# Performance work log

Hardware: AMD Instinct MI355X
Metric: run time of the kernel (lower is better)

## Reference

```python
import jax, jax.numpy as jnp
import numpy as np

NUM_FEATURES = 81   # atom feature width used in matmuls
N_NODES = 262144
N_COLS = 103        # num_features + num_bond
OUT_CH = 128
COORD = 3           # distance rule slice [0:3]


def setup_inputs() -> dict:
    key = jax.random.key(0)
    k1, k2, k3, k4 = jax.random.split(key, 4)
    features = jax.random.normal(k1, (N_NODES, N_COLS), dtype=jnp.float32)
    # columns 81, 82 hold neighbor indices (0 => no neighbor), stored as floats
    idx = jax.random.randint(k4, (N_NODES, 2), 0, N_NODES).astype(jnp.float32)
    features = features.at[:, NUM_FEATURES:NUM_FEATURES + 2].set(idx)
    w_s = jax.random.normal(k2, (NUM_FEATURES, OUT_CH), dtype=jnp.float32) * 0.05
    w_n = jax.random.normal(k3, (N_COLS, OUT_CH), dtype=jnp.float32) * 0.05
    return {"features": features, "w_s": w_s, "w_n": w_n}


def reference(features, w_s, w_n):
    F = NUM_FEATURES
    self_f = features[:, :F]                       # [N, F]
    new_features = self_f @ w_s                    # [N, C] self term

    idx0 = features[:, F].astype(jnp.int32)        # neighbor slot 0
    idx1 = features[:, F + 1].astype(jnp.int32)    # neighbor slot 1

    def neighbor_contrib(idx):
        nei = features[idx]                                        # gather [N, 103]
        # rule 0: 'distance' over [0:COORD] -> keep neighbor slice, record distance
        d = jnp.sqrt(jnp.sum(jnp.square(self_f[:, :COORD] - nei[:, :COORD]), axis=-1))
        seg_dist = nei[:, :COORD]                                  # [N, 3]
        # rule 1: 'sum' over [COORD:F]
        seg_sum = self_f[:, COORD:F] + nei[:, COORD:F]             # [N, F-3]
        comb = jnp.concatenate([seg_dist, seg_sum], axis=-1)       # [N, F]
        d_eff = jnp.where(d > 0, d, jnp.float32(0.01))
        comb = comb / jnp.square(d_eff)[:, None]                   # distance scaling
        return comb @ w_n[:F] + new_features                       # tiny-matmul batched

    c0 = neighbor_contrib(idx0)
    c1 = neighbor_contrib(idx1)
    # rows with no valid neighbor were never written -> zeros
    out = jnp.where((idx1 != 0)[:, None], c1,
                    jnp.where((idx0 != 0)[:, None], c0, jnp.float32(0.0)))
    return out
```

## Files before the change

### kernel.cpp

```cpp
#include <hip/hip_runtime.h>
#include <hip/hip_bf16.h>

constexpr int kNodes = 262144;
constexpr int NC  = 103;
constexpr int F   = 81;
constexpr int OC  = 128;
constexpr int NKS = 6;
constexpr int NPB = 64;
constexpr int THREADS = 256;
constexpr int NST = 96;
constexpr int SELF_F4 = NPB * NC / 4;

typedef __attribute__((ext_vector_type(8))) short bf16x8;
typedef __attribute__((ext_vector_type(4))) float f32x4;

__device__ inline ushort f2bf(float f) {
  uint u = __float_as_uint(f);
  return (ushort)((u + 0x7fffu + ((u >> 16) & 1u)) >> 16);
}
__device__ inline short bfc(float x) {
  return (short)__bfloat16_as_ushort(__float2bfloat16(x));
}

__device__ __forceinline__ void gll4(const float* g, float* l) {
  __builtin_amdgcn_global_load_lds(
      (const __attribute__((address_space(1))) unsigned int*)g,
      (__attribute__((address_space(3))) unsigned int*)l, 4, 0, 0);
}
__device__ __forceinline__ void gll16(const float* g, float* l) {
  __builtin_amdgcn_global_load_lds(
      (const __attribute__((address_space(1))) unsigned int*)g,
      (__attribute__((address_space(3))) unsigned int*)l, 16, 0, 0);
}

__global__ __launch_bounds__(256)
void prep_w(const float* __restrict__ w_s, const float* __restrict__ w_n,
            ushort* __restrict__ wf) {
  int t = blockIdx.x * 256 + threadIdx.x;
  if (t >= NKS * 8 * 64) return;
  int l  = t & 63;
  int ct = (t >> 6) & 7;
  int ks = t >> 9;
  int c  = ct * 16 + (l & 15);
  int kb = ks * 32 + ((l >> 4) << 3);
  union { ushort u[8]; int4 v; } o;
  #pragma unroll
  for (int i = 0; i < 8; ++i) {
    int k = kb + i;
    float f = 0.f;
    if (k < F)                      f = w_s[k * OC + c];
    else if (k >= 96 && k < 96 + F) f = w_n[(k - 96) * OC + c];
    o.u[i] = f2bf(f);
  }
  ((int4*)wf)[t] = o.v;
}

__global__ __launch_bounds__(THREADS)
void rgc_v13(const float* __restrict__ feat, const ushort* __restrict__ wf,
             float* __restrict__ out) {
  __shared__ __align__(16) float lds_self[NPB * NC];
  __shared__ __align__(16) float lds_nei[NPB * NST];
  __shared__ int   s_sel[NPB];
  __shared__ float s_cs[NPB];

  const int tid = threadIdx.x;
  const int w   = tid >> 6;
  const int l   = tid & 63;
  const long base = (long)blockIdx.x * NPB;
  const float* fbase = feat + base * NC;

  const bf16x8* wfv = (const bf16x8*)wf;
  bf16x8 bA[NKS], bB[NKS];
  #pragma unroll
  for (int ks = 0; ks < NKS; ++ks) {
    bA[ks] = wfv[(ks * 8 + w)     * 64 + l];
    bB[ks] = wfv[(ks * 8 + w + 4) * 64 + l];
  }

  #pragma unroll
  for (int j = 0; j < 7; ++j) {
    int i = tid + j * THREADS;
    if (j < 6 || i < SELF_F4) {
      gll16((const float*)((const float4*)fbase + i),
            (float*)((float4*)lds_self + (j * THREADS + w * 64)));
    }
  }
  if (l < 16) {
    const int n = w * 16 + l;
    const float* row = feat + (base + n) * NC;
    float f0 = row[F], f1 = row[F + 1];
    int i0 = (int)f0, i1 = (int)f1;
    s_sel[n] = (i1 != 0) ? i1 : i0;
  }
  asm volatile("s_waitcnt lgkmcnt(0)" ::: "memory");
  __builtin_amdgcn_s_barrier();

  #pragma unroll
  for (int j = 0; j < 24; ++j) {
    int v   = tid + j * THREADS;
    int row = v / NST;
    int p   = v - row * NST;
    int c   = p >> 5;
    int x   = (p >> 2) & 7;
    int cl  = p & 3;
    int col = (c << 5) + ((x ^ (row & 7)) << 2) + cl;
    gll4(feat + (long)s_sel[row] * NC + col,
         lds_nei + (j * THREADS + w * 64));
  }
  asm volatile("s_waitcnt vmcnt(0) lgkmcnt(0)" ::: "memory");
  __builtin_amdgcn_s_barrier();

  if (tid < NPB) {
    const int n = tid;
    const int r = n & 7;
    float nx = lds_nei[n * NST + r * 4 + 0];
    float ny = lds_nei[n * NST + r * 4 + 1];
    float nz = lds_nei[n * NST + r * 4 + 2];
    float dx = lds_self[n * NC + 0] - nx;
    float dy = lds_self[n * NC + 1] - ny;
    float dz = lds_self[n * NC + 2] - nz;
    float d2 = dx * dx + dy * dy + dz * dz;
    float alive = (s_sel[n] != 0) ? 1.f : 0.f;
    s_cs[n] = alive * ((d2 > 0.f) ? (1.f / d2) : 10000.f);
  }
  asm volatile("s_waitcnt lgkmcnt(0)" ::: "memory");
  __builtin_amdgcn_s_barrier();

  const int q    = l >> 4;
  const int lrow = l & 15;
  const int off0 = q * 8;
  const int col  = l & 15;

  #pragma unroll
  for (int nt = 0; nt < 4; ++nt) {
    const int n = nt * 16 + lrow;
    const int r = n & 7;
    const float* sp = lds_self + n * NC;
    const float* np = lds_nei + n * NST;
    const float alive = (s_sel[n] != 0) ? 1.f : 0.f;
    const float cs    = s_cs[n];

    bf16x8 afS[3], afC[3];
    #pragma unroll
    for (int c = 0; c < 3; ++c) {
      f32x4 lo = *(const f32x4*)(np + c * 32 + (((2 * q)     ^ r) << 2));
      f32x4 hi = *(const f32x4*)(np + c * 32 + (((2 * q + 1) ^ r) << 2));
      #pragma unroll
      for (int i = 0; i < 8; ++i) {
        float sv = sp[c * 32 + off0 + i];
        float nv = (i < 4) ? lo[i] : hi[i - 4];
        afS[c][i] = bfc(sv * alive);
        float se = sv;
        if (c == 0 && i < 3 && q == 0) se = 0.f;
        afC[c][i] = bfc((nv + se) * cs);
      }
    }

    f32x4 a0 = (f32x4)(0.f), a1 = (f32x4)(0.f);
    #pragma unroll
    for (int ks = 0; ks < NKS; ++ks) {
      bf16x8 af = (ks < 3) ? afS[ks] : afC[ks - 3];
      a0 = __builtin_amdgcn_mfma_f32_16x16x32_bf16(af, bA[ks], a0, 0, 0, 0);
      a1 = __builtin_amdgcn_mfma_f32_16x16x32_bf16(af, bB[ks], a1, 0, 0, 0);
    }

    const long orow = base + nt * 16 + q * 4;
    #pragma unroll
    for (int rr = 0; rr < 4; ++rr) {
      out[(orow + rr) * OC + w * 16       + col] = a0[rr];
      out[(orow + rr) * OC + (w + 4) * 16 + col] = a1[rr];
    }
  }
}

extern "C" void kernel_launch(void* const* d_in, const int* in_sizes, int n_in,
                              void* d_out, int out_size, void* d_ws, size_t ws_size,
                              hipStream_t stream) {
  const float* feat = (const float*)d_in[0];
  const float* w_s  = (const float*)d_in[1];
  const float* w_n  = (const float*)d_in[2];
  float* outp = (float*)d_out;
  ushort* wf = (ushort*)d_ws;

  prep_w<<<dim3((NKS * 8 * 64 + 255) / 256), 256, 0, stream>>>(w_s, w_n, wf);
  rgc_v13<<<dim3(kNodes / NPB), THREADS, 0, stream>>>(feat, wf, outp);
}
```

Before: 67.75 us.

## Read self rows directly from global into registers, drop self LDS staging

Removes the LDS staging buffer for the block's own feature rows. Each lane now loads its 24 self features straight from global memory as unaligned 4-wide vectors, and computes the distance scale per lane instead of in a separate pass with an extra barrier. This cuts LDS footprint, which may raise occupancy, and removes one barrier phase. The cost is uncoalesced, redundant global reads of the self rows, since four waves read the same rows, and the node-tile loop is no longer unrolled.

```diff
diff --git a/kernel.cpp b/kernel.cpp
--- a/kernel.cpp
+++ b/kernel.cpp
@@ -9,10 +9,10 @@
 constexpr int NPB = 64;
 constexpr int THREADS = 256;
 constexpr int NST = 96;
-constexpr int SELF_F4 = NPB * NC / 4;
 
 typedef __attribute__((ext_vector_type(8))) short bf16x8;
 typedef __attribute__((ext_vector_type(4))) float f32x4;
+typedef float f32x4u __attribute__((ext_vector_type(4))) __attribute__((aligned(4)));
 
 __device__ inline ushort f2bf(float f) {
   uint u = __float_as_uint(f);
@@ -26,11 +26,6 @@
   __builtin_amdgcn_global_load_lds(
       (const __attribute__((address_space(1))) unsigned int*)g,
       (__attribute__((address_space(3))) unsigned int*)l, 4, 0, 0);
-}
-__device__ __forceinline__ void gll16(const float* g, float* l) {
-  __builtin_amdgcn_global_load_lds(
-      (const __attribute__((address_space(1))) unsigned int*)g,
-      (__attribute__((address_space(3))) unsigned int*)l, 16, 0, 0);
 }
 
 __global__ __launch_bounds__(256)
@@ -56,18 +51,15 @@
 }
 
 __global__ __launch_bounds__(THREADS)
-void rgc_v13(const float* __restrict__ feat, const ushort* __restrict__ wf,
+void rgc_v14(const float* __restrict__ feat, const ushort* __restrict__ wf,
              float* __restrict__ out) {
-  __shared__ __align__(16) float lds_self[NPB * NC];
   __shared__ __align__(16) float lds_nei[NPB * NST];
-  __shared__ int   s_sel[NPB];
-  __shared__ float s_cs[NPB];
+  __shared__ int s_sel[NPB];
 
   const int tid = threadIdx.x;
   const int w   = tid >> 6;
   const int l   = tid & 63;
   const long base = (long)blockIdx.x * NPB;
-  const float* fbase = feat + base * NC;
 
   const bf16x8* wfv = (const bf16x8*)wf;
   bf16x8 bA[NKS], bB[NKS];
@@ -77,14 +69,6 @@
     bB[ks] = wfv[(ks * 8 + w + 4) * 64 + l];
   }
 
-  #pragma unroll
-  for (int j = 0; j < 7; ++j) {
-    int i = tid + j * THREADS;
-    if (j < 6 || i < SELF_F4) {
-      gll16((const float*)((const float4*)fbase + i),
-            (float*)((float4*)lds_self + (j * THREADS + w * 64)));
-    }
-  }
   if (l < 16) {
     const int n = w * 16 + l;
     const float* row = feat + (base + n) * NC;
@@ -107,23 +91,7 @@
     gll4(feat + (long)s_sel[row] * NC + col,
          lds_nei + (j * THREADS + w * 64));
   }
-  asm volatile("s_waitcnt vmcnt(0) lgkmcnt(0)" ::: "memory");
-  __builtin_amdgcn_s_barrier();
-
-  if (tid < NPB) {
-    const int n = tid;
-    const int r = n & 7;
-    float nx = lds_nei[n * NST + r * 4 + 0];
-    float ny = lds_nei[n * NST + r * 4 + 1];
-    float nz = lds_nei[n * NST + r * 4 + 2];
-    float dx = lds_self[n * NC + 0] - nx;
-    float dy = lds_self[n * NC + 1] - ny;
-    float dz = lds_self[n * NC + 2] - nz;
-    float d2 = dx * dx + dy * dy + dz * dz;
-    float alive = (s_sel[n] != 0) ? 1.f : 0.f;
-    s_cs[n] = alive * ((d2 > 0.f) ? (1.f / d2) : 10000.f);
-  }
-  asm volatile("s_waitcnt lgkmcnt(0)" ::: "memory");
+  asm volatile("s_waitcnt vmcnt(0)" ::: "memory");
   __builtin_amdgcn_s_barrier();
 
   const int q    = l >> 4;
@@ -131,14 +99,29 @@
   const int off0 = q * 8;
   const int col  = l & 15;
 
-  #pragma unroll
+  #pragma unroll 1
   for (int nt = 0; nt < 4; ++nt) {
     const int n = nt * 16 + lrow;
     const int r = n & 7;
-    const float* sp = lds_self + n * NC;
-    const float* np = lds_nei + n * NST;
-    const float alive = (s_sel[n] != 0) ? 1.f : 0.f;
-    const float cs    = s_cs[n];
+    const float* srow = feat + (base + n) * NC;
+    const float* np   = lds_nei + n * NST;
+    const int sel     = s_sel[n];
+    const float alive = (sel != 0) ? 1.f : 0.f;
+
+    f32x4u s8[3][2];
+    #pragma unroll
+    for (int c = 0; c < 3; ++c) {
+      s8[c][0] = *(const f32x4u*)(srow + c * 32 + off0);
+      s8[c][1] = *(const f32x4u*)(srow + c * 32 + off0 + 4);
+    }
+    float sc0 = srow[0], sc1 = srow[1], sc2 = srow[2];
+
+    float nx = np[(r << 2) + 0];
+    float ny = np[(r << 2) + 1];
+    float nz = np[(r << 2) + 2];
+    float dx = sc0 - nx, dy = sc1 - ny, dz = sc2 - nz;
+    float d2 = dx * dx + dy * dy + dz * dz;
+    float cs = alive * ((d2 > 0.f) ? (1.f / d2) : 10000.f);
 
     bf16x8 afS[3], afC[3];
     #pragma unroll
@@ -147,7 +130,7 @@
       f32x4 hi = *(const f32x4*)(np + c * 32 + (((2 * q + 1) ^ r) << 2));
       #pragma unroll
       for (int i = 0; i < 8; ++i) {
-        float sv = sp[c * 32 + off0 + i];
+        float sv = s8[c][i >> 2][i & 3];
         float nv = (i < 4) ? lo[i] : hi[i - 4];
         afS[c][i] = bfc(sv * alive);
         float se = sv;
@@ -183,5 +166,5 @@
   ushort* wf = (ushort*)d_ws;
 
   prep_w<<<dim3((NKS * 8 * 64 + 255) / 256), 256, 0, stream>>>(w_s, w_n, wf);
-  rgc_v13<<<dim3(kNodes / NPB), THREADS, 0, stream>>>(feat, wf, outp);
+  rgc_v14<<<dim3(kNodes / NPB), THREADS, 0, stream>>>(feat, wf, outp);
 }
```

Measured after the change: 78.96 us. 16.5% more time.
